# Kernel optimization log

Measured on AMD Instinct MI355X. Metric: run time of the kernel, lower is better.

The kernel has to match this reference:

```python
import jax, jax.numpy as jnp
import numpy as np

S, XD, C, R = 6, 3, 8, 64   # num_freqs, x_dim, num_channels, res_scale
N = 262144
STD = 0.001


def setup_inputs() -> dict:
    key = jax.random.key(0)
    k1, k2, k3 = jax.random.split(key, 3)
    x = jax.random.uniform(k1, (N, XD), dtype=jnp.float32)
    features = jax.random.normal(k2, (S, 2 * XD, C, R, R), dtype=jnp.float32) * STD
    features_2d = jax.random.normal(k3, (S, 2 * XD, C, R, R), dtype=jnp.float32) * STD
    return {"x": x, "features": features, "features_2d": features_2d}


def _bilinear(img, gx, gy):
    # img: [C,H,W]; gx,gy: [P] normalized coords in [-1,1]
    # bilinear grid_sample, align_corners=True, clamped (border) indices
    _, H, W = img.shape
    ix = (gx + 1.0) * 0.5 * (W - 1)
    iy = (gy + 1.0) * 0.5 * (H - 1)
    ix0f = jnp.floor(ix)
    iy0f = jnp.floor(iy)
    wx = ix - ix0f
    wy = iy - iy0f
    ix0 = jnp.clip(ix0f.astype(jnp.int32), 0, W - 1)
    iy0 = jnp.clip(iy0f.astype(jnp.int32), 0, H - 1)
    ix1 = jnp.clip(ix0 + 1, 0, W - 1)
    iy1 = jnp.clip(iy0 + 1, 0, H - 1)
    v00 = img[:, iy0, ix0]  # [C,P]
    v01 = img[:, iy0, ix1]
    v10 = img[:, iy1, ix0]
    v11 = img[:, iy1, ix1]
    return (v00 * (1 - wx) * (1 - wy) + v01 * wx * (1 - wy)
            + v10 * (1 - wx) * wy + v11 * wx * wy)


def reference(x, features, features_2d):
    n = x.shape[0]
    scales = 2.0 ** jnp.arange(S, dtype=x.dtype)                   # [S]
    xb = x[:, None, :] * scales[:, None]                           # [N,S,3]
    latent = jnp.sin(jnp.stack([xb, xb + 0.5 * jnp.pi], axis=-2))  # [N,S,2,3]

    B = S * 2 * XD  # 36 independent (scale, sin/cos, dim) lookups

    # 1D (line) lookup: grid x-coord fixed at 0, y-coord = encoded value
    gy = jnp.transpose(latent.reshape(n, S, 2 * XD), (1, 2, 0)).reshape(B, n)
    gx = jnp.zeros_like(gy)
    fs = jax.vmap(_bilinear)(features.reshape(B, C, R, R), gx, gy)  # [B,C,N]
    fs = fs.reshape(S, 2, XD, C, n)

    # 2D (plane) lookup with cyclic dim pairs (1,2),(2,0),(0,1)
    pairs = jnp.array([[1, 2], [2, 0], [0, 1]])
    g2 = latent[..., pairs]                                        # [N,S,2,3,2]
    gx2 = jnp.transpose(g2[..., 0], (1, 2, 3, 0)).reshape(B, n)
    gy2 = jnp.transpose(g2[..., 1], (1, 2, 3, 0)).reshape(B, n)
    fs2 = jax.vmap(_bilinear)(features_2d.reshape(B, C, R, R), gx2, gy2)
    fs2 = fs2.reshape(S, 2, XD, C, n)

    out = jnp.transpose(fs * fs2, (4, 3, 0, 1, 2))                 # [N,C,S,2,3]
    out = out + latent[:, None]                                    # + PE, broadcast over C
    return out.reshape(n, C * S * 2 * XD)                          # [N, 288]
```

## Files before the change

### kernel.cpp

```cpp
#include <hip/hip_runtime.h>

#define NS 6
#define NXD 3
#define NC 8
#define NR 64
#define NB 36
#define NPOINTS 262144
#define OUTD 288
#define PTS 32

__device__ __forceinline__ unsigned short f2bf(float f) {
    unsigned u = __float_as_uint(f);
    unsigned r = u + 0x7fffu + ((u >> 16) & 1u);
    return (unsigned short)(r >> 16);
}
__device__ __forceinline__ unsigned pack2(float a, float b) {
    return (unsigned)f2bf(a) | ((unsigned)f2bf(b) << 16);
}

__global__ void build_px(const float* __restrict__ F2, unsigned* __restrict__ px) {
    int tid = blockIdx.x * 256 + threadIdx.x;
    const int total = NB * 65 * 64 * NC;
    if (tid >= total) return;
    int c = tid & 7;
    int xx = (tid >> 3) & 63;
    int rest = tid >> 9;
    int y = rest % 65;
    int b = rest / 65;
    int ys = y < 63 ? y : 63;
    const float* src = F2 + (((size_t)(b * NC + c) * NR + ys) * NR);
    float v0 = src[xx];
    float v1 = src[xx < 63 ? xx + 1 : 63];
    px[tid] = pack2(v0, v1);
}

__global__ void build_f1q(const float* __restrict__ F, unsigned* __restrict__ f1q) {
    int tid = blockIdx.x * 256 + threadIdx.x;
    const int total = NB * 64 * NC;
    if (tid >= total) return;
    int c = tid & 7;
    int y = (tid >> 3) & 63;
    int b = tid >> 9;
    const float* img = F + (size_t)(b * NC + c) * NR * NR;
    float a = 0.5f * (img[y * NR + 31] + img[y * NR + 32]);
    int y1 = y < 63 ? y + 1 : 63;
    float bb = 0.5f * (img[y1 * NR + 31] + img[y1 * NR + 32]);
    f1q[tid] = pack2(a, bb);
}

__global__ __launch_bounds__(256, 3) void encode_kernel(
    const float* __restrict__ x,
    const unsigned* __restrict__ px,
    const unsigned* __restrict__ f1q,
    float* __restrict__ out)
{
    __shared__ float lat[PTS][NB];
    __shared__ float stage[PTS * 289];
    const int t = threadIdx.x;
    const int c = t & 7;
    const int u = t >> 3;
    const int n = blockIdx.x * PTS + u;

    const float xv0 = x[3 * n + 0];
    const float xv1 = x[3 * n + 1];
    const float xv2 = x[3 * n + 2];

    #pragma unroll
    for (int ii = 0; ii < 5; ++ii) {
        int i = c + ii * 8;
        if (i < NB) {
            int s = i / 6;
            int rr = i - s * 6;
            int p = rr / 3;
            int d = rr - p * 3;
            float xb = (d == 0 ? xv0 : (d == 1 ? xv1 : xv2)) * (float)(1 << s);
            lat[u][i] = p ? __cosf(xb) : __sinf(xb);
        }
    }
    __syncthreads();

    const float* latu = lat[u];
    float* stg = &stage[u * 289];

    for (int g = 0; g < 12; ++g) {
        const int b0 = g * 3;
        #pragma unroll
        for (int k = 0; k < 3; ++k) {
            const int b = b0 + k;
            const int i0 = b0 + (k == 0 ? 1 : (k == 1 ? 2 : 0));
            const int i1 = b0 + (k == 0 ? 2 : (k == 1 ? 0 : 1));
            float gy1 = latu[b];
            float ga = latu[i0];
            float gb = latu[i1];

            float fy = fminf(fmaxf(__builtin_fmaf(gy1, 31.5f, 31.5f), 0.0f), 63.0f);
            float fy0 = floorf(fy);
            float wy = fy - fy0;
            int y0 = (int)fy0;
            unsigned pr = f1q[(b * 64 + y0) * 8 + c];
            float a0 = __uint_as_float(pr << 16);
            float a1 = __uint_as_float(pr & 0xffff0000u);
            float fsv = __builtin_fmaf(a1 - a0, wy, a0);

            float fx2 = fminf(fmaxf(__builtin_fmaf(ga, 31.5f, 31.5f), 0.0f), 63.0f);
            float fy2 = fminf(fmaxf(__builtin_fmaf(gb, 31.5f, 31.5f), 0.0f), 63.0f);
            float fx20 = floorf(fx2);
            float fy20 = floorf(fy2);
            float wx2 = fx2 - fx20;
            float wy2 = fy2 - fy20;
            int xx = (int)fx20;
            int yy = (int)fy20;
            const unsigned* rb = px + ((b * 65 + yy) * 64 + xx) * 8 + c;
            unsigned top = rb[0];
            unsigned bot = rb[512];
            float v00 = __uint_as_float(top << 16);
            float v01 = __uint_as_float(top & 0xffff0000u);
            float v10 = __uint_as_float(bot << 16);
            float v11 = __uint_as_float(bot & 0xffff0000u);
            float tp = __builtin_fmaf(v01 - v00, wx2, v00);
            float bt = __builtin_fmaf(v11 - v10, wx2, v10);
            float fs2v = __builtin_fmaf(bt - tp, wy2, tp);

            stg[c * 36 + b] = __builtin_fmaf(fsv, fs2v, gy1);
        }
    }
    __syncthreads();

    float* ob = out + (size_t)blockIdx.x * (PTS * OUTD);
    #pragma unroll
    for (int r = 0; r < 36; ++r) {
        int e = t + r * 256;
        int uu = e / 288;
        int v = e - uu * 288;
        ob[e] = stage[uu * 289 + v];
    }
}

extern "C" void kernel_launch(void* const* d_in, const int* in_sizes, int n_in,
                              void* d_out, int out_size, void* d_ws, size_t ws_size,
                              hipStream_t stream)
{
    const float* x  = (const float*)d_in[0];
    const float* F  = (const float*)d_in[1];
    const float* F2 = (const float*)d_in[2];
    float* out = (float*)d_out;

    unsigned* px  = (unsigned*)d_ws;
    unsigned* f1q = px + NB * 65 * 64 * NC;

    build_px<<<(NB * 65 * 64 * NC + 255) / 256, 256, 0, stream>>>(F2, px);
    build_f1q<<<(NB * 64 * NC + 255) / 256, 256, 0, stream>>>(F, f1q);
    encode_kernel<<<NPOINTS / PTS, 256, 0, stream>>>(x, px, f1q, out);
}
```

Measured before the change: 399.4 us.

## Pack bilinear quads, compute latents in registers, store outputs directly

Adds a table that stores all four bilinear neighbours (bf16 packed into a uint2), so each 2D lookup becomes one 8-byte gather instead of two 4-byte gathers, with a fallback when workspace is too small. The shared-memory latent table and output staging buffer are removed. Each thread now computes its own sin/cos and writes its 36 contiguous outputs with non-temporal float4 stores. This drops two block barriers and the LDS traffic, at the cost of a table twice as large and output stores that are less coalesced across the wave, since each thread writes a 144-byte run.

```diff
diff --git a/kernel.cpp b/kernel.cpp
--- a/kernel.cpp
+++ b/kernel.cpp
@@ -9,6 +9,8 @@
 #define OUTD 288
 #define PTS 32
 
+typedef float vfloat4 __attribute__((ext_vector_type(4)));
+
 __device__ __forceinline__ unsigned short f2bf(float f) {
     unsigned u = __float_as_uint(f);
     unsigned r = u + 0x7fffu + ((u >> 16) & 1u);
@@ -18,11 +20,25 @@
     return (unsigned)f2bf(a) | ((unsigned)f2bf(b) << 16);
 }
 
-__global__ void build_px(const float* __restrict__ F2, unsigned* __restrict__ px) {
+__global__ void build_pxq(const float* __restrict__ F2, uint2* __restrict__ pxq) {
+    int tid = blockIdx.x * 256 + threadIdx.x;
+    int c  = tid & 7;
+    int xx = (tid >> 3) & 63;
+    int y  = (tid >> 9) & 63;
+    int b  = tid >> 15;
+    const float* img = F2 + (size_t)(b * NC + c) * NR * NR;
+    int x1 = xx < 63 ? xx + 1 : 63;
+    int y1 = y  < 63 ? y  + 1 : 63;
+    float v00 = img[y  * 64 + xx], v01 = img[y  * 64 + x1];
+    float v10 = img[y1 * 64 + xx], v11 = img[y1 * 64 + x1];
+    pxq[tid] = make_uint2(pack2(v00, v01), pack2(v10, v11));
+}
+
+__global__ void build_px65(const float* __restrict__ F2, unsigned* __restrict__ px) {
     int tid = blockIdx.x * 256 + threadIdx.x;
     const int total = NB * 65 * 64 * NC;
     if (tid >= total) return;
-    int c = tid & 7;
+    int c  = tid & 7;
     int xx = (tid >> 3) & 63;
     int rest = tid >> 9;
     int y = rest % 65;
@@ -48,14 +64,13 @@
     f1q[tid] = pack2(a, bb);
 }
 
-__global__ __launch_bounds__(256, 3) void encode_kernel(
+template <bool QUAD>
+__global__ __launch_bounds__(256) void encode_kernel(
     const float* __restrict__ x,
-    const unsigned* __restrict__ px,
+    const void* __restrict__ pxv,
     const unsigned* __restrict__ f1q,
     float* __restrict__ out)
 {
-    __shared__ float lat[PTS][NB];
-    __shared__ float stage[PTS * 289];
     const int t = threadIdx.x;
     const int c = t & 7;
     const int u = t >> 3;
@@ -65,74 +80,67 @@
     const float xv1 = x[3 * n + 1];
     const float xv2 = x[3 * n + 2];
 
+    float o[NB];
+
     #pragma unroll
-    for (int ii = 0; ii < 5; ++ii) {
-        int i = c + ii * 8;
-        if (i < NB) {
-            int s = i / 6;
-            int rr = i - s * 6;
-            int p = rr / 3;
-            int d = rr - p * 3;
-            float xb = (d == 0 ? xv0 : (d == 1 ? xv1 : xv2)) * (float)(1 << s);
-            lat[u][i] = p ? __cosf(xb) : __sinf(xb);
-        }
-    }
-    __syncthreads();
-
-    const float* latu = lat[u];
-    float* stg = &stage[u * 289];
-
     for (int g = 0; g < 12; ++g) {
-        const int b0 = g * 3;
+        const int s = g >> 1;
+        const int p = g & 1;
+        const float sc = (float)(1 << s);
+        float l0, l1, l2;
+        if (p == 0) { l0 = __sinf(xv0 * sc); l1 = __sinf(xv1 * sc); l2 = __sinf(xv2 * sc); }
+        else        { l0 = __cosf(xv0 * sc); l1 = __cosf(xv1 * sc); l2 = __cosf(xv2 * sc); }
+        const float la[3] = {l0, l1, l2};
         #pragma unroll
         for (int k = 0; k < 3; ++k) {
-            const int b = b0 + k;
-            const int i0 = b0 + (k == 0 ? 1 : (k == 1 ? 2 : 0));
-            const int i1 = b0 + (k == 0 ? 2 : (k == 1 ? 0 : 1));
-            float gy1 = latu[b];
-            float ga = latu[i0];
-            float gb = latu[i1];
+            const int b = g * 3 + k;
+            const float gy1 = la[k];
+            const float ga  = la[k == 0 ? 1 : (k == 1 ? 2 : 0)];
+            const float gb  = la[k == 0 ? 2 : (k == 1 ? 0 : 1)];
 
-            float fy = fminf(fmaxf(__builtin_fmaf(gy1, 31.5f, 31.5f), 0.0f), 63.0f);
+            float fy  = fminf(fmaxf(__builtin_fmaf(gy1, 31.5f, 31.5f), 0.0f), 63.0f);
             float fy0 = floorf(fy);
-            float wy = fy - fy0;
-            int y0 = (int)fy0;
+            float wy  = fy - fy0;
+            int   y0  = (int)fy0;
             unsigned pr = f1q[(b * 64 + y0) * 8 + c];
             float a0 = __uint_as_float(pr << 16);
             float a1 = __uint_as_float(pr & 0xffff0000u);
             float fsv = __builtin_fmaf(a1 - a0, wy, a0);
 
             float fx2 = fminf(fmaxf(__builtin_fmaf(ga, 31.5f, 31.5f), 0.0f), 63.0f);
-            float fy2 = fminf(fmaxf(__builtin_fmaf(gb, 31.5f, 31.5f), 0.0f), 63.0f);
-            float fx20 = floorf(fx2);
-            float fy20 = floorf(fy2);
-            float wx2 = fx2 - fx20;
-            float wy2 = fy2 - fy20;
-            int xx = (int)fx20;
-            int yy = (int)fy20;
-            const unsigned* rb = px + ((b * 65 + yy) * 64 + xx) * 8 + c;
-            unsigned top = rb[0];
-            unsigned bot = rb[512];
-            float v00 = __uint_as_float(top << 16);
-            float v01 = __uint_as_float(top & 0xffff0000u);
-            float v10 = __uint_as_float(bot << 16);
-            float v11 = __uint_as_float(bot & 0xffff0000u);
-            float tp = __builtin_fmaf(v01 - v00, wx2, v00);
-            float bt = __builtin_fmaf(v11 - v10, wx2, v10);
+            float fyy = fminf(fmaxf(__builtin_fmaf(gb, 31.5f, 31.5f), 0.0f), 63.0f);
+            float fx0 = floorf(fx2), fyy0 = floorf(fyy);
+            float wx  = fx2 - fx0,   wy2  = fyy - fyy0;
+            int   xx  = (int)fx0,    yy   = (int)fyy0;
+
+            unsigned qx, qy;
+            if (QUAD) {
+                const uint2* pxq = (const uint2*)pxv;
+                uint2 q = pxq[b * 32768 + (yy * 64 + xx) * 8 + c];
+                qx = q.x; qy = q.y;
+            } else {
+                const unsigned* px = (const unsigned*)pxv;
+                const unsigned* rb = px + ((b * 65 + yy) * 64 + xx) * 8 + c;
+                qx = rb[0];
+                qy = rb[512];
+            }
+            float v00 = __uint_as_float(qx << 16);
+            float v01 = __uint_as_float(qx & 0xffff0000u);
+            float v10 = __uint_as_float(qy << 16);
+            float v11 = __uint_as_float(qy & 0xffff0000u);
+            float tp   = __builtin_fmaf(v01 - v00, wx, v00);
+            float bt   = __builtin_fmaf(v11 - v10, wx, v10);
             float fs2v = __builtin_fmaf(bt - tp, wy2, tp);
 
-            stg[c * 36 + b] = __builtin_fmaf(fsv, fs2v, gy1);
+            o[b] = __builtin_fmaf(fsv, fs2v, gy1);
         }
     }
-    __syncthreads();
 
-    float* ob = out + (size_t)blockIdx.x * (PTS * OUTD);
+    vfloat4* ob = (vfloat4*)(out + (size_t)n * OUTD + c * 36);
     #pragma unroll
-    for (int r = 0; r < 36; ++r) {
-        int e = t + r * 256;
-        int uu = e / 288;
-        int v = e - uu * 288;
-        ob[e] = stage[uu * 289 + v];
+    for (int q = 0; q < 9; ++q) {
+        vfloat4 v = {o[4 * q + 0], o[4 * q + 1], o[4 * q + 2], o[4 * q + 3]};
+        __builtin_nontemporal_store(v, ob + q);
     }
 }
 
@@ -145,10 +153,19 @@
     const float* F2 = (const float*)d_in[2];
     float* out = (float*)d_out;
 
-    unsigned* px  = (unsigned*)d_ws;
-    unsigned* f1q = px + NB * 65 * 64 * NC;
+    const size_t quad_bytes = (size_t)NB * 64 * 64 * NC * 8 + (size_t)NB * 64 * NC * 4;
 
-    build_px<<<(NB * 65 * 64 * NC + 255) / 256, 256, 0, stream>>>(F2, px);
-    build_f1q<<<(NB * 64 * NC + 255) / 256, 256, 0, stream>>>(F, f1q);
-    encode_kernel<<<NPOINTS / PTS, 256, 0, stream>>>(x, px, f1q, out);
+    if (ws_size >= quad_bytes) {
+        uint2* pxq    = (uint2*)d_ws;
+        unsigned* f1q = (unsigned*)(pxq + NB * 64 * 64 * NC);
+        build_pxq<<<NB * 64 * 64 * NC / 256, 256, 0, stream>>>(F2, pxq);
+        build_f1q<<<(NB * 64 * NC + 255) / 256, 256, 0, stream>>>(F, f1q);
+        encode_kernel<true><<<NPOINTS / PTS, 256, 0, stream>>>(x, pxq, f1q, out);
+    } else {
+        unsigned* px  = (unsigned*)d_ws;
+        unsigned* f1q = px + NB * 65 * 64 * NC;
+        build_px65<<<(NB * 65 * 64 * NC + 255) / 256, 256, 0, stream>>>(F2, px);
+        build_f1q<<<(NB * 64 * NC + 255) / 256, 256, 0, stream>>>(F, f1q);
+        encode_kernel<false><<<NPOINTS / PTS, 256, 0, stream>>>(x, px, f1q, out);
+    }
 }
```

Result: slower. 881.3 us (+120.6%).
